# Performance work log

Measured on AMD Instinct MI355X. Metric: run time of the kernel, lower is better.

Reference implementation:

```python
import jax, jax.numpy as jnp
import numpy as np

Q_LORA = 1536
KV_LORA = 512
ROPE_DIM = 64
NOPE_DIM = 128
NUM_HEADS = 16
QK_HEAD_DIM = NOPE_DIM + ROPE_DIM  # 192
HEAD_SIZE = KV_LORA + ROPE_DIM     # 576
MAX_POS = 4096
ROPE_BASE = 10000.0
T = 32768


def _rope_cos_sin(positions):
    # inv_freq: [ROPE_DIM//2]
    inv_freq = 1.0 / (ROPE_BASE ** (jnp.arange(0, ROPE_DIM, 2, dtype=jnp.float32) / ROPE_DIM))
    freqs = positions.astype(jnp.float32)[:, None] * inv_freq[None, :]  # [T, D/2]
    return jnp.cos(freqs), jnp.sin(freqs)


def _apply_rope_neox(x, cos, sin):
    # x: [T, H, D]; cos/sin: [T, D/2] broadcast over heads
    x1, x2 = jnp.split(x, 2, axis=-1)
    c = cos[:, None, :]
    s = sin[:, None, :]
    return jnp.concatenate([x1 * c - x2 * s, x2 * c + x1 * s], axis=-1)


def setup_inputs() -> dict:
    key = jax.random.key(0)
    k1, k2, k3 = jax.random.split(key, 3)
    qkv_lora = jax.random.normal(k1, (T, Q_LORA + KV_LORA + ROPE_DIM), dtype=jnp.float32)
    positions = jax.random.randint(k2, (T,), 0, MAX_POS, dtype=jnp.int64)
    Wq = jax.random.normal(k3, (Q_LORA, NUM_HEADS * QK_HEAD_DIM), dtype=jnp.float32) * 0.02
    kv_cache = jnp.zeros((T, HEAD_SIZE), dtype=jnp.float32)
    slot_mapping = jnp.arange(T, dtype=jnp.int64)
    return {"qkv_lora": qkv_lora, "positions": positions, "Wq": Wq,
            "kv_cache": kv_cache, "slot_mapping": slot_mapping}


def reference(qkv_lora, positions, Wq, kv_cache, slot_mapping):
    # split low-rank projections
    q_c = qkv_lora[:, :Q_LORA]                               # [T, 1536]
    kv_c = qkv_lora[:, Q_LORA:Q_LORA + KV_LORA]              # [T, 512]
    k_pe = qkv_lora[:, Q_LORA + KV_LORA:]                    # [T, 64]

    # q_b_proj GEMM then reshape to heads
    q = (q_c @ Wq).reshape(T, NUM_HEADS, QK_HEAD_DIM)        # [T, H, 192]

    # RoPE on q rope slice and k_pe (neox style)
    cos, sin = _rope_cos_sin(positions)
    q_pe = _apply_rope_neox(q[..., NOPE_DIM:], cos, sin)     # [T, H, 64]
    k_pe_rot = _apply_rope_neox(k_pe[:, None, :], cos, sin)  # [T, 1, 64]
    q = jnp.concatenate([q[..., :NOPE_DIM], q_pe], axis=-1)

    # paged KV cache scatter write: concat(kv_c, k_pe) at slot_mapping
    entry = jnp.concatenate([kv_c, k_pe_rot[:, 0, :]], axis=-1)  # [T, 576]
    kv_cache = kv_cache.at[slot_mapping].set(entry)

    return q, kv_c, k_pe_rot, kv_cache
```

## Files before the change

### kernel.cpp

```cpp
#include <hip/hip_runtime.h>
#include <hip/hip_bf16.h>
#include <stdint.h>

typedef unsigned short ushort_t;
typedef __attribute__((ext_vector_type(4))) float f32x4;
typedef __attribute__((ext_vector_type(8))) short short8;

#define T_TOK 32768
#define QL    1536
#define KVL   512
#define RD    64
#define NQ    3072
#define ROWW  2112
#define HS    576

#define BM 256
#define BN 256
#define BK 64
#define KT (QL / BK)
#define MT (T_TOK / BM)
#define NT (NQ / BN)

#define ACONV_BLOCKS (T_TOK * 192 / 256)
#define WQ_BLOCKS    ((NQ / 32) * (QL / 32))
#define KVP_BLOCKS   (T_TOK / 4)

#define NLOG (-0.28782313662425572f)

static __device__ __forceinline__ short f2bf(float x) {
  __hip_bfloat16 h = __float2bfloat16(x);
  return *reinterpret_cast<short*>(&h);
}

#define NTST(p, v) __builtin_nontemporal_store((v), (p))

#define GLOAD16(gp, lp)                                        \
  __builtin_amdgcn_global_load_lds(                            \
      (const __attribute__((address_space(1))) void*)(gp),     \
      (__attribute__((address_space(3))) void*)(lp), 16, 0, 0)

static __device__ __forceinline__ void kv_body(
    int tok, int lane, const float* __restrict__ qkv, const int* __restrict__ pos,
    const int* __restrict__ slots, float* __restrict__ out_kvc,
    float* __restrict__ out_kpe, float* __restrict__ out_cache) {
  const float* src = qkv + (size_t)tok * ROWW + QL;
  float* dkv = out_kvc + (size_t)tok * KVL;
  float* dc  = out_cache + (size_t)slots[tok] * HS;
#pragma unroll
  for (int i = 0; i < 2; ++i) {
    f32x4 v = *(const f32x4*)(src + (size_t)(lane + 64 * i) * 4);
    NTST((f32x4*)(dkv + (size_t)(lane + 64 * i) * 4), v);
    NTST((f32x4*)(dc + (size_t)(lane + 64 * i) * 4), v);
  }
  if (lane < 32) {
    float x1 = src[KVL + lane], x2 = src[KVL + 32 + lane];
    float p = (float)pos[tok];
    float invf = __expf((float)lane * NLOG);
    float s, c;
    __sincosf(p * invf, &s, &c);
    float r1 = x1 * c - x2 * s;
    float r2 = x2 * c + x1 * s;
    NTST(out_kpe + (size_t)tok * RD + lane, r1);
    NTST(out_kpe + (size_t)tok * RD + 32 + lane, r2);
    NTST(dc + KVL + lane, r1);
    NTST(dc + KVL + 32 + lane, r2);
  }
}

__global__ __launch_bounds__(256) void pre_kernel(
    const float* __restrict__ qkv, ushort_t* __restrict__ Abf,
    const float* __restrict__ Wq, ushort_t* __restrict__ Wt,
    const int* __restrict__ pos, const int* __restrict__ slots,
    float* __restrict__ out_kvc, float* __restrict__ out_kpe,
    float* __restrict__ out_cache, int do_kv) {
  __shared__ float tile[32][33];
  int bid = blockIdx.x, tid = threadIdx.x;
  if (bid < ACONV_BLOCKS) {
    int g = bid * 256 + tid;
    int row = g / 192;
    int col = (g - row * 192) * 8;
    const float* s = qkv + (size_t)row * ROWW + col;
    f32x4 a = *(const f32x4*)s;
    f32x4 b = *(const f32x4*)(s + 4);
    short8 v;
    v[0] = f2bf(a[0]); v[1] = f2bf(a[1]); v[2] = f2bf(a[2]); v[3] = f2bf(a[3]);
    v[4] = f2bf(b[0]); v[5] = f2bf(b[1]); v[6] = f2bf(b[2]); v[7] = f2bf(b[3]);
    *(short8*)(Abf + (size_t)row * QL + col) = v;
  } else if (bid < ACONV_BLOCKS + WQ_BLOCKS) {
    int b2 = bid - ACONV_BLOCKS;
    int n0 = (b2 % (NQ / 32)) * 32, k0 = (b2 / (NQ / 32)) * 32;
    int tx = tid & 31, ty = tid >> 5;
#pragma unroll
    for (int j = 0; j < 32; j += 8)
      tile[ty + j][tx] = Wq[(size_t)(k0 + ty + j) * NQ + n0 + tx];
    __syncthreads();
#pragma unroll
    for (int j = 0; j < 32; j += 8)
      Wt[(size_t)(n0 + ty + j) * QL + k0 + tx] = f2bf(tile[tx][ty + j]);
  } else if (do_kv) {
    int b3 = bid - ACONV_BLOCKS - WQ_BLOCKS;
    int tok = b3 * 4 + (tid >> 6);
    kv_body(tok, tid & 63, qkv, pos, slots, out_kvc, out_kpe, out_cache);
  }
}

__global__ __launch_bounds__(512, 2) void gemm_rope_kernel(
    const ushort_t* __restrict__ Abf, const int* __restrict__ pos,
    const ushort_t* __restrict__ wt, float* __restrict__ out_q) {
  __shared__ ushort_t lds[2][2][2][256 * 32];

  int bid = blockIdx.x;
  int vb = (bid & 7) * (MT * NT / 8) + (bid >> 3);
  int m0 = (vb / NT) * BM;
  int n0 = (vb % NT) * BN;

  int tid = threadIdx.x;
  int wv = tid >> 6, ln = tid & 63;
  int l16 = ln & 15, lq4 = ln >> 4;
  int wm = wv >> 2, wn = wv & 3;

  int srow = wv * 32 + (ln >> 2);
  int schunk = ((ln & 3) ^ ((ln >> 3) & 3)) * 8;
  const ushort_t* aS = Abf + (size_t)(m0 + srow) * QL + schunk;
  const ushort_t* bS = wt  + (size_t)(n0 + srow) * QL + schunk;
  int sdst = wv * 32 * 32;

#define STG(PAR, AB, KH, TT, SRC) do {                                         \
    GLOAD16((SRC) + (size_t)(TT) * BK + (KH) * 32,           &lds[PAR][AB][KH][sdst]);       \
    GLOAD16((SRC) + (size_t)(TT) * BK + (KH) * 32 + 16 * QL, &lds[PAR][AB][KH][sdst + 512]); \
  } while (0)

  int rkey = (l16 >> 1) & 3;
  int aoff = (wm * 128 + l16) * 32 + (lq4 ^ rkey) * 8;
  int boff = (wn * 64  + l16) * 32 + (lq4 ^ rkey) * 8;

  f32x4 acc[8][4];
#pragma unroll
  for (int i = 0; i < 8; ++i)
#pragma unroll
    for (int j = 0; j < 4; ++j) acc[i][j] = (f32x4)0.0f;

  STG(0, 0, 0, 0, aS);
  STG(0, 1, 0, 0, bS);
  STG(0, 0, 1, 0, aS);
  STG(0, 1, 1, 0, bS);
  STG(1, 0, 0, 1, aS);
  STG(1, 1, 0, 1, bS);

#define CLUSTER(ACCBASE, AF, BF)                                               \
  __builtin_amdgcn_s_setprio(1);                                               \
  _Pragma("unroll")                                                            \
  for (int q = 0; q < 4; ++q)                                                  \
    _Pragma("unroll")                                                          \
    for (int n = 0; n < 4; ++n)                                                \
      acc[(ACCBASE) + q][n] = __builtin_amdgcn_mfma_f32_16x16x32_bf16(         \
          AF[q], BF[n], acc[(ACCBASE) + q][n], 0, 0, 0);                       \
  __builtin_amdgcn_s_setprio(0);

#pragma unroll 2
  for (int t = 0; t < KT; ++t) {
    int par = t & 1;
    const ushort_t* Ak0 = &lds[par][0][0][0];
    const ushort_t* Bk0 = &lds[par][1][0][0];
    const ushort_t* Ak1 = &lds[par][0][1][0];
    const ushort_t* Bk1 = &lds[par][1][1][0];
    short8 af0[4], af1[4], bf0[4], ag0[4], ag1[4], bg0[4];

    __builtin_amdgcn_sched_barrier(0);
    if (t == KT - 1) { asm volatile("s_waitcnt vmcnt(0)" ::: "memory"); }
    else             { asm volatile("s_waitcnt vmcnt(4)" ::: "memory"); }
    __builtin_amdgcn_s_barrier();
    __builtin_amdgcn_sched_barrier(0);

#pragma unroll
    for (int q = 0; q < 4; ++q) af0[q] = *(const short8*)(Ak0 + aoff + q * 512);
#pragma unroll
    for (int n = 0; n < 4; ++n) bf0[n] = *(const short8*)(Bk0 + boff + n * 512);
#pragma unroll
    for (int q = 0; q < 4; ++q) af1[q] = *(const short8*)(Ak0 + aoff + (4 + q) * 512);
    if (t + 1 < KT) { STG(par ^ 1, 0, 1, t + 1, aS); STG(par ^ 1, 1, 1, t + 1, bS); }

    CLUSTER(0, af0, bf0)
    CLUSTER(4, af1, bf0)

#pragma unroll
    for (int q = 0; q < 4; ++q) ag0[q] = *(const short8*)(Ak1 + aoff + q * 512);
#pragma unroll
    for (int n = 0; n < 4; ++n) bg0[n] = *(const short8*)(Bk1 + boff + n * 512);
#pragma unroll
    for (int q = 0; q < 4; ++q) ag1[q] = *(const short8*)(Ak1 + aoff + (4 + q) * 512);

    __builtin_amdgcn_sched_barrier(0);
    __builtin_amdgcn_s_barrier();
    __builtin_amdgcn_sched_barrier(0);
    if (t + 2 < KT) { STG(par, 0, 0, t + 2, aS); STG(par, 1, 0, t + 2, bS); }

    CLUSTER(0, ag0, bg0)
    CLUSTER(4, ag1, bg0)
  }

  int gn = n0 + wn * 64;
  bool ropew = ((gn % 192) == 128);
  if (!ropew) {
#pragma unroll
    for (int mi = 0; mi < 8; ++mi)
#pragma unroll
      for (int r = 0; r < 4; ++r) {
        int t = m0 + wm * 128 + mi * 16 + lq4 * 4 + r;
        float* rowp = out_q + (size_t)t * NQ + gn + l16;
        NTST(rowp + 0,  acc[mi][0][r]);
        NTST(rowp + 16, acc[mi][1][r]);
        NTST(rowp + 32, acc[mi][2][r]);
        NTST(rowp + 48, acc[mi][3][r]);
      }
  } else {
    float invf0 = __expf((float)l16 * NLOG);
    float invf1 = __expf((float)(l16 + 16) * NLOG);
#pragma unroll
    for (int mi = 0; mi < 8; ++mi)
#pragma unroll
      for (int r = 0; r < 4; ++r) {
        int t = m0 + wm * 128 + mi * 16 + lq4 * 4 + r;
        float p = (float)pos[t];
        float s0, c0, s1, c1;
        __sincosf(p * invf0, &s0, &c0);
        __sincosf(p * invf1, &s1, &c1);
        float x1a = acc[mi][0][r], x1b = acc[mi][1][r];
        float x2a = acc[mi][2][r], x2b = acc[mi][3][r];
        float* rowp = out_q + (size_t)t * NQ + gn + l16;
        NTST(rowp + 0,  x1a * c0 - x2a * s0);
        NTST(rowp + 16, x1b * c1 - x2b * s1);
        NTST(rowp + 32, x2a * c0 + x1a * s0);
        NTST(rowp + 48, x2b * c1 + x1b * s1);
      }
  }
}

__global__ void kv_kernel(const float* __restrict__ qkv, const int* __restrict__ pos,
                          const int* __restrict__ slots,
                          float* __restrict__ out_kvc, float* __restrict__ out_kpe,
                          float* __restrict__ out_cache) {
  int tok = blockIdx.x * 4 + (threadIdx.x >> 6);
  kv_body(tok, threadIdx.x & 63, qkv, pos, slots, out_kvc, out_kpe, out_cache);
}

extern "C" void kernel_launch(void* const* d_in, const int* in_sizes, int n_in,
                              void* d_out, int out_size, void* d_ws, size_t ws_size,
                              hipStream_t stream) {
  const float* qkv       = (const float*)d_in[0];
  const int*   positions = (const int*)d_in[1];
  const float* Wq        = (const float*)d_in[2];
  const int*   slots     = (const int*)d_in[4];

  float* out_q     = (float*)d_out;
  float* out_kvc   = out_q   + (size_t)T_TOK * NQ;
  float* out_kpe   = out_kvc + (size_t)T_TOK * KVL;
  float* out_cache = out_kpe + (size_t)T_TOK * RD;

  size_t abf_bytes = (size_t)T_TOK * QL * sizeof(ushort_t);
  size_t wt_bytes  = (size_t)NQ * QL * sizeof(ushort_t);
  int ws_ok = (ws_size >= abf_bytes + wt_bytes);
  char* scratch = ws_ok ? (char*)d_ws : (char*)out_kvc;
  ushort_t* Abf = (ushort_t*)scratch;
  ushort_t* Wt  = (ushort_t*)(scratch + abf_bytes);

  int pre_blocks = ACONV_BLOCKS + WQ_BLOCKS + (ws_ok ? KVP_BLOCKS : 0);
  pre_kernel<<<dim3(pre_blocks), dim3(256), 0, stream>>>(
      qkv, Abf, Wq, Wt, positions, slots, out_kvc, out_kpe, out_cache, ws_ok);
  gemm_rope_kernel<<<dim3(MT * NT), dim3(512), 0, stream>>>(Abf, positions, Wt, out_q);
  if (!ws_ok)
    kv_kernel<<<dim3(KVP_BLOCKS), dim3(256), 0, stream>>>(qkv, positions, slots,
                                                          out_kvc, out_kpe, out_cache);
}
```

Before: 415.8 us.

## Make GEMM blocks persistent over six N tiles with cross-tile prefetch

Each GEMM block now loops over six consecutive N tiles for one M tile, launching 256 blocks instead of 1536. The first K-stages of the next tile are prefetched during the tail of the current tile, so the pipeline does not drain and refill between tiles, and launch overhead and the tail effect are reduced. The costs are fewer blocks (256 on a large-CU GPU, which may leave some CUs idle or unbalanced), repeated reads of the A rows that now depend on L2, and delicate vmcnt accounting across the epilogue stores.

```diff
diff --git a/kernel.cpp b/kernel.cpp
--- a/kernel.cpp
+++ b/kernel.cpp
@@ -20,6 +20,7 @@
 #define KT (QL / BK)
 #define MT (T_TOK / BM)
 #define NT (NQ / BN)
+#define TPB 6
 
 #define ACONV_BLOCKS (T_TOK * 192 / 256)
 #define WQ_BLOCKS    ((NQ / 32) * (QL / 32))
@@ -110,9 +111,9 @@
   __shared__ ushort_t lds[2][2][2][256 * 32];
 
   int bid = blockIdx.x;
-  int vb = (bid & 7) * (MT * NT / 8) + (bid >> 3);
-  int m0 = (vb / NT) * BM;
-  int n0 = (vb % NT) * BN;
+  int cid = (bid & 7) * 32 + (bid >> 3);
+  int m0 = (cid >> 1) * BM;
+  int nbase = (cid & 1) * TPB;
 
   int tid = threadIdx.x;
   int wv = tid >> 6, ln = tid & 63;
@@ -122,7 +123,6 @@
   int srow = wv * 32 + (ln >> 2);
   int schunk = ((ln & 3) ^ ((ln >> 3) & 3)) * 8;
   const ushort_t* aS = Abf + (size_t)(m0 + srow) * QL + schunk;
-  const ushort_t* bS = wt  + (size_t)(n0 + srow) * QL + schunk;
   int sdst = wv * 32 * 32;
 
 #define STG(PAR, AB, KH, TT, SRC) do {                                         \
@@ -133,19 +133,6 @@
   int rkey = (l16 >> 1) & 3;
   int aoff = (wm * 128 + l16) * 32 + (lq4 ^ rkey) * 8;
   int boff = (wn * 64  + l16) * 32 + (lq4 ^ rkey) * 8;
-
-  f32x4 acc[8][4];
-#pragma unroll
-  for (int i = 0; i < 8; ++i)
-#pragma unroll
-    for (int j = 0; j < 4; ++j) acc[i][j] = (f32x4)0.0f;
-
-  STG(0, 0, 0, 0, aS);
-  STG(0, 1, 0, 0, bS);
-  STG(0, 0, 1, 0, aS);
-  STG(0, 1, 1, 0, bS);
-  STG(1, 0, 0, 1, aS);
-  STG(1, 1, 0, 1, bS);
 
 #define CLUSTER(ACCBASE, AF, BF)                                               \
   __builtin_amdgcn_s_setprio(1);                                               \
@@ -157,82 +144,111 @@
           AF[q], BF[n], acc[(ACCBASE) + q][n], 0, 0, 0);                       \
   __builtin_amdgcn_s_setprio(0);
 
+  f32x4 acc[8][4];
+
+  {
+    const ushort_t* bS0 = wt + (size_t)((nbase) * BN + srow) * QL + schunk;
+    STG(0, 0, 0, 0, aS);
+    STG(0, 1, 0, 0, bS0);
+    STG(0, 0, 1, 0, aS);
+    STG(0, 1, 1, 0, bS0);
+    STG(1, 0, 0, 1, aS);
+    STG(1, 1, 0, 1, bS0);
+  }
+
+  for (int j = 0; j < TPB; ++j) {
+    int n0 = (nbase + j) * BN;
+    const ushort_t* bS  = wt + (size_t)(n0 + srow) * QL + schunk;
+    const ushort_t* bSn = wt + (size_t)(n0 + BN + srow) * QL + schunk;
+    const bool last = (j == TPB - 1);
+
+#pragma unroll
+    for (int i = 0; i < 8; ++i)
+#pragma unroll
+      for (int jj = 0; jj < 4; ++jj) acc[i][jj] = (f32x4)0.0f;
+
 #pragma unroll 2
-  for (int t = 0; t < KT; ++t) {
-    int par = t & 1;
-    const ushort_t* Ak0 = &lds[par][0][0][0];
-    const ushort_t* Bk0 = &lds[par][1][0][0];
-    const ushort_t* Ak1 = &lds[par][0][1][0];
-    const ushort_t* Bk1 = &lds[par][1][1][0];
-    short8 af0[4], af1[4], bf0[4], ag0[4], ag1[4], bg0[4];
-
-    __builtin_amdgcn_sched_barrier(0);
-    if (t == KT - 1) { asm volatile("s_waitcnt vmcnt(0)" ::: "memory"); }
-    else             { asm volatile("s_waitcnt vmcnt(4)" ::: "memory"); }
-    __builtin_amdgcn_s_barrier();
-    __builtin_amdgcn_sched_barrier(0);
-
-#pragma unroll
-    for (int q = 0; q < 4; ++q) af0[q] = *(const short8*)(Ak0 + aoff + q * 512);
-#pragma unroll
-    for (int n = 0; n < 4; ++n) bf0[n] = *(const short8*)(Bk0 + boff + n * 512);
-#pragma unroll
-    for (int q = 0; q < 4; ++q) af1[q] = *(const short8*)(Ak0 + aoff + (4 + q) * 512);
-    if (t + 1 < KT) { STG(par ^ 1, 0, 1, t + 1, aS); STG(par ^ 1, 1, 1, t + 1, bS); }
-
-    CLUSTER(0, af0, bf0)
-    CLUSTER(4, af1, bf0)
-
-#pragma unroll
-    for (int q = 0; q < 4; ++q) ag0[q] = *(const short8*)(Ak1 + aoff + q * 512);
-#pragma unroll
-    for (int n = 0; n < 4; ++n) bg0[n] = *(const short8*)(Bk1 + boff + n * 512);
-#pragma unroll
-    for (int q = 0; q < 4; ++q) ag1[q] = *(const short8*)(Ak1 + aoff + (4 + q) * 512);
-
-    __builtin_amdgcn_sched_barrier(0);
-    __builtin_amdgcn_s_barrier();
-    __builtin_amdgcn_sched_barrier(0);
-    if (t + 2 < KT) { STG(par, 0, 0, t + 2, aS); STG(par, 1, 0, t + 2, bS); }
-
-    CLUSTER(0, ag0, bg0)
-    CLUSTER(4, ag1, bg0)
-  }
-
-  int gn = n0 + wn * 64;
-  bool ropew = ((gn % 192) == 128);
-  if (!ropew) {
-#pragma unroll
-    for (int mi = 0; mi < 8; ++mi)
-#pragma unroll
-      for (int r = 0; r < 4; ++r) {
-        int t = m0 + wm * 128 + mi * 16 + lq4 * 4 + r;
-        float* rowp = out_q + (size_t)t * NQ + gn + l16;
-        NTST(rowp + 0,  acc[mi][0][r]);
-        NTST(rowp + 16, acc[mi][1][r]);
-        NTST(rowp + 32, acc[mi][2][r]);
-        NTST(rowp + 48, acc[mi][3][r]);
-      }
-  } else {
-    float invf0 = __expf((float)l16 * NLOG);
-    float invf1 = __expf((float)(l16 + 16) * NLOG);
-#pragma unroll
-    for (int mi = 0; mi < 8; ++mi)
-#pragma unroll
-      for (int r = 0; r < 4; ++r) {
-        int t = m0 + wm * 128 + mi * 16 + lq4 * 4 + r;
-        float p = (float)pos[t];
-        float s0, c0, s1, c1;
-        __sincosf(p * invf0, &s0, &c0);
-        __sincosf(p * invf1, &s1, &c1);
-        float x1a = acc[mi][0][r], x1b = acc[mi][1][r];
-        float x2a = acc[mi][2][r], x2b = acc[mi][3][r];
-        float* rowp = out_q + (size_t)t * NQ + gn + l16;
-        NTST(rowp + 0,  x1a * c0 - x2a * s0);
-        NTST(rowp + 16, x1b * c1 - x2b * s1);
-        NTST(rowp + 32, x2a * c0 + x1a * s0);
-        NTST(rowp + 48, x2b * c1 + x1b * s1);
-      }
+    for (int t = 0; t < KT; ++t) {
+      int par = t & 1;
+      const ushort_t* Ak0 = &lds[par][0][0][0];
+      const ushort_t* Bk0 = &lds[par][1][0][0];
+      const ushort_t* Ak1 = &lds[par][0][1][0];
+      const ushort_t* Bk1 = &lds[par][1][1][0];
+      short8 af0[4], af1[4], bf0[4], ag0[4], ag1[4], bg0[4];
+
+      __builtin_amdgcn_sched_barrier(0);
+      if (last && t == KT - 1) { asm volatile("s_waitcnt vmcnt(0)" ::: "memory"); }
+      else                     { asm volatile("s_waitcnt vmcnt(4)" ::: "memory"); }
+      __builtin_amdgcn_s_barrier();
+      __builtin_amdgcn_sched_barrier(0);
+
+#pragma unroll
+      for (int q = 0; q < 4; ++q) af0[q] = *(const short8*)(Ak0 + aoff + q * 512);
+#pragma unroll
+      for (int n = 0; n < 4; ++n) bf0[n] = *(const short8*)(Bk0 + boff + n * 512);
+#pragma unroll
+      for (int q = 0; q < 4; ++q) af1[q] = *(const short8*)(Ak0 + aoff + (4 + q) * 512);
+      if (t + 1 < KT)      { STG(par ^ 1, 0, 1, t + 1, aS); STG(par ^ 1, 1, 1, t + 1, bS); }
+      else if (!last)      { STG(par ^ 1, 0, 1, 0, aS);     STG(par ^ 1, 1, 1, 0, bSn); }
+
+      CLUSTER(0, af0, bf0)
+      CLUSTER(4, af1, bf0)
+
+#pragma unroll
+      for (int q = 0; q < 4; ++q) ag0[q] = *(const short8*)(Ak1 + aoff + q * 512);
+#pragma unroll
+      for (int n = 0; n < 4; ++n) bg0[n] = *(const short8*)(Bk1 + boff + n * 512);
+#pragma unroll
+      for (int q = 0; q < 4; ++q) ag1[q] = *(const short8*)(Ak1 + aoff + (4 + q) * 512);
+
+      __builtin_amdgcn_sched_barrier(0);
+      __builtin_amdgcn_s_barrier();
+      __builtin_amdgcn_sched_barrier(0);
+      if (t + 2 < KT)      { STG(par, 0, 0, t + 2, aS); STG(par, 1, 0, t + 2, bS); }
+      else if (!last)      { int tn = t + 2 - KT;
+                             STG(par, 0, 0, tn, aS);   STG(par, 1, 0, tn, bSn); }
+
+      CLUSTER(0, ag0, bg0)
+      CLUSTER(4, ag1, bg0)
+    }
+
+    int gn = n0 + wn * 64;
+    bool ropew = ((gn % 192) == 128);
+    if (!ropew) {
+#pragma unroll
+      for (int mi = 0; mi < 8; ++mi)
+#pragma unroll
+        for (int r = 0; r < 4; ++r) {
+          int t = m0 + wm * 128 + mi * 16 + lq4 * 4 + r;
+          float* rowp = out_q + (size_t)t * NQ + gn + l16;
+          NTST(rowp + 0,  acc[mi][0][r]);
+          NTST(rowp + 16, acc[mi][1][r]);
+          NTST(rowp + 32, acc[mi][2][r]);
+          NTST(rowp + 48, acc[mi][3][r]);
+        }
+    } else {
+      float invf0 = __expf((float)l16 * NLOG);
+      float invf1 = __expf((float)(l16 + 16) * NLOG);
+#pragma unroll
+      for (int mi = 0; mi < 8; ++mi)
+#pragma unroll
+        for (int r = 0; r < 4; ++r) {
+          int t = m0 + wm * 128 + mi * 16 + lq4 * 4 + r;
+          float p = (float)pos[t];
+          float s0, c0, s1, c1;
+          __sincosf(p * invf0, &s0, &c0);
+          __sincosf(p * invf1, &s1, &c1);
+          float x1a = acc[mi][0][r], x1b = acc[mi][1][r];
+          float x2a = acc[mi][2][r], x2b = acc[mi][3][r];
+          float* rowp = out_q + (size_t)t * NQ + gn + l16;
+          NTST(rowp + 0,  x1a * c0 - x2a * s0);
+          NTST(rowp + 16, x1b * c1 - x2b * s1);
+          NTST(rowp + 32, x2a * c0 + x1a * s0);
+          NTST(rowp + 48, x2b * c1 + x1b * s1);
+        }
+    }
+
+    if (!last) { asm volatile("s_waitcnt vmcnt(12)" ::: "memory"); }
   }
 }
 
@@ -267,7 +283,8 @@
   int pre_blocks = ACONV_BLOCKS + WQ_BLOCKS + (ws_ok ? KVP_BLOCKS : 0);
   pre_kernel<<<dim3(pre_blocks), dim3(256), 0, stream>>>(
       qkv, Abf, Wq, Wt, positions, slots, out_kvc, out_kpe, out_cache, ws_ok);
-  gemm_rope_kernel<<<dim3(MT * NT), dim3(512), 0, stream>>>(Abf, positions, Wt, out_q);
+  gemm_rope_kernel<<<dim3(MT * NT / TPB), dim3(512), 0, stream>>>(
+      Abf, positions, Wt, out_q);
   if (!ws_ok)
     kv_kernel<<<dim3(KVP_BLOCKS), dim3(256), 0, stream>>>(qkv, positions, slots,
                                                           out_kvc, out_kpe, out_cache);
```

New measurement: 489.9 us. +17.8%, slower.
